# Performance work log

Hardware: AMD Instinct MI355X
Metric: run time of the kernel (lower is better)

The kernel has to match this reference:

```python
import jax, jax.numpy as jnp
import numpy as np

N = 100000       # nodes
E = 1600000      # edges (before self loops)
G = 64           # graphs in batch
IN, HID, OUT = 128, 64, 16
NEG_SLOPE = 0.2  # PyG GATConv default


def setup_inputs() -> dict:
    key = jax.random.key(0)
    ks = jax.random.split(key, 16)
    s = 0.1  # weight init scale
    return {
        "x": jax.random.normal(ks[0], (N, IN), dtype=jnp.float32),
        "edge_index": jax.random.randint(ks[1], (2, E), 0, N, dtype=jnp.int32),
        "batch": jnp.sort(jax.random.randint(ks[2], (N,), 0, G, dtype=jnp.int32)),
        "W1": jax.random.normal(ks[3], (IN, 2 * HID), dtype=jnp.float32) * s,
        "a_src1": jax.random.normal(ks[4], (2, HID), dtype=jnp.float32) * s,
        "a_dst1": jax.random.normal(ks[5], (2, HID), dtype=jnp.float32) * s,
        "b1": jax.random.normal(ks[6], (2 * HID,), dtype=jnp.float32) * s,
        "W2": jax.random.normal(ks[7], (2 * HID, HID), dtype=jnp.float32) * s,
        "a_src2": jax.random.normal(ks[8], (1, HID), dtype=jnp.float32) * s,
        "a_dst2": jax.random.normal(ks[9], (1, HID), dtype=jnp.float32) * s,
        "b2": jax.random.normal(ks[10], (HID,), dtype=jnp.float32) * s,
        "dw1": jax.random.normal(ks[11], (HID, HID), dtype=jnp.float32) * s,
        "db1": jax.random.normal(ks[12], (HID,), dtype=jnp.float32) * s,
        "dw2": jax.random.normal(ks[13], (HID, OUT), dtype=jnp.float32) * s,
        "db2": jax.random.normal(ks[14], (OUT,), dtype=jnp.float32) * s,
    }


def gat_conv(x, src, dst, W, a_src, a_dst, b):
    """PyG GATConv (concat=True, self-loops already appended to src/dst)."""
    n = x.shape[0]
    heads, out = a_src.shape
    h = (x @ W).reshape(n, heads, out)                       # [N,H,O]
    e_src = jnp.einsum("nho,ho->nh", h, a_src)               # [N,H]
    e_dst = jnp.einsum("nho,ho->nh", h, a_dst)
    e = jax.nn.leaky_relu(e_src[src] + e_dst[dst], NEG_SLOPE)  # [E',H]
    # segment softmax over incoming edges of each destination node
    m = jax.lax.stop_gradient(jax.ops.segment_max(e, dst, num_segments=n))
    a = jnp.exp(e - m[dst])
    denom = jax.ops.segment_sum(a, dst, num_segments=n)
    alpha = a / denom[dst]                                   # [E',H]
    msg = h[src] * alpha[:, :, None]                         # [E',H,O]
    agg = jax.ops.segment_sum(msg, dst, num_segments=n)      # [N,H,O]
    return agg.reshape(n, heads * out) + b


def reference(x, edge_index, batch, W1, a_src1, a_dst1, b1, W2, a_src2, a_dst2,
              b2, dw1, db1, dw2, db2):
    n = x.shape[0]
    loops = jnp.arange(n, dtype=edge_index.dtype)            # add_self_loops=True
    src = jnp.concatenate([edge_index[0], loops])
    dst = jnp.concatenate([edge_index[1], loops])

    h = jax.nn.relu(gat_conv(x, src, dst, W1, a_src1, a_dst1, b1))   # [N,128]
    h = gat_conv(h, src, dst, W2, a_src2, a_dst2, b2)                # [N,64]

    # global mean pool over graphs
    cnt = jax.ops.segment_sum(jnp.ones((n,), h.dtype), batch, num_segments=G)
    pooled = jax.ops.segment_sum(h, batch, num_segments=G)
    pooled = pooled / jnp.maximum(cnt, 1.0)[:, None]                  # [G,64]

    # decoder MLP (dropout inactive in eval)
    z = jax.nn.relu(pooled @ dw1 + db1)
    return z @ dw2 + db2                                              # [G,16]
```

## Files before the change

### kernel.cpp

```cpp
#include <hip/hip_runtime.h>
#include <stdint.h>


#define LRELU(x) ((x) > 0.f ? (x) : 0.2f * (x))
#define LOG2E 1.4426950408889634f
#define BCAP 3072
#define PSLICE 8

typedef short bf8 __attribute__((ext_vector_type(8)));
typedef float f32x4 __attribute__((ext_vector_type(4)));
typedef float f32x2 __attribute__((ext_vector_type(2)));

__device__ __forceinline__ uint16_t f2bf(float f) {
  uint32_t u = __float_as_uint(f);
  u += 0x7fff + ((u >> 16) & 1);
  return (uint16_t)(u >> 16);
}
__device__ __forceinline__ uint32_t pack2bf(float a, float b) {
  return (uint32_t)f2bf(a) | ((uint32_t)f2bf(b) << 16);
}
__device__ __forceinline__ uint8_t f2fp8(float v) {
  return (uint8_t)(__builtin_amdgcn_cvt_pk_fp8_f32(v, v, 0, false) & 0xff);
}
__device__ __forceinline__ void fp8x4_to_f32(uint32_t v, float* o) {
  f32x2 lo = __builtin_amdgcn_cvt_pk_f32_fp8(v, false);
  f32x2 hi = __builtin_amdgcn_cvt_pk_f32_fp8(v, true);
  o[0] = lo[0]; o[1] = lo[1]; o[2] = hi[0]; o[3] = hi[1];
}
__device__ __forceinline__ void a1_edge(const uint4& gv, float av, float* acc) {
  float f[16];
  fp8x4_to_f32(gv.x, f);     fp8x4_to_f32(gv.y, f + 4);
  fp8x4_to_f32(gv.z, f + 8); fp8x4_to_f32(gv.w, f + 12);
#pragma unroll
  for (int j = 0; j < 16; ++j) acc[j] = fmaf(av, f[j], acc[j]);
}
__device__ __forceinline__ void a2_edge(const uint2& gv, float av, float* acc) {
  float f[8];
  fp8x4_to_f32(gv.x, f); fp8x4_to_f32(gv.y, f + 4);
#pragma unroll
  for (int j = 0; j < 8; ++j) acc[j] = fmaf(av, f[j], acc[j]);
}


__global__ __launch_bounds__(256) void scatter_cvt_kernel(
    const int* __restrict__ ei, int* __restrict__ bcur,
    uint32_t* __restrict__ bpack, const float* __restrict__ W1,
    const float* __restrict__ W2, uint16_t* __restrict__ WT1,
    uint16_t* __restrict__ WT2, int E, int E2, int shift, int nb, int gCH) {
  int blk = blockIdx.x;
  int t = threadIdx.x;
  if (blk >= gCH) {
    int idx = (blk - gCH) * 256 + t;
    if (idx < 128 * 128) {
      int n = idx >> 7, k = idx & 127;
      WT1[idx] = f2bf(W1[(size_t)k * 128 + n]);
    } else if (idx < 128 * 128 + 64 * 128) {
      int j = idx - 128 * 128;
      int n = j >> 7, k = j & 127;
      WT2[j] = f2bf(W2[(size_t)k * 64 + n]);
    }
    return;
  }
  __shared__ int lh[1024];
  __shared__ int lb[1024];
  for (int i = t; i < 1024; i += 256) lh[i] = 0;
  __syncthreads();
  int base = blk * 4096;
  int bszm1 = (1 << shift) - 1;
  uint32_t pk[16];
  int rk[16], bk[16];
#pragma unroll
  for (int u = 0; u < 16; ++u) {
    int e = base + u * 256 + t;
    if (e < E2) {
      int s, d;
      if (e < E) { s = ei[e]; d = ei[E + e]; } else { s = d = e - E; }
      bk[u] = d >> shift;
      pk[u] = ((uint32_t)s << shift) | (uint32_t)(d & bszm1);
      rk[u] = atomicAdd(&lh[bk[u]], 1);
    } else rk[u] = -1;
  }
  __syncthreads();
  for (int i = t; i < nb; i += 256) {
    int c = lh[i];
    lb[i] = c ? atomicAdd(&bcur[i], c) : 0;
  }
  __syncthreads();
#pragma unroll
  for (int u = 0; u < 16; ++u) {
    if (rk[u] >= 0) {
      int pos = lb[bk[u]] + rk[u];
      if (pos < BCAP) bpack[(size_t)bk[u] * BCAP + pos] = pk[u];
    }
  }
}


__device__ __forceinline__ void bfinal_body(const uint32_t* __restrict__ bpack,
                                            const int* __restrict__ bcur,
                                            int2* __restrict__ off2,
                                            int* __restrict__ ssrc, int N,
                                            int shift, int b) {
  __shared__ int hist[512];
  __shared__ int loff[512];
  __shared__ int ssc[256];
  __shared__ int lsrc[BCAP];
  int t = threadIdx.x;
  int bsz = 1 << shift;
  int node0 = b << shift;
  int e0 = b * BCAP;
  int cnt = min(bcur[b], BCAP);
  for (int i = t; i < bsz; i += 256) hist[i] = 0;
  __syncthreads();
  uint32_t pe[12];
  int ne = 0;
#pragma unroll
  for (int j = 0; j < 12; ++j) {
    int i = j * 256 + t;
    if (i < cnt) { pe[j] = bpack[(size_t)b * BCAP + i]; ne = j + 1; }
  }
  int bszm1 = bsz - 1;
  for (int j = 0; j < ne; ++j) atomicAdd(&hist[pe[j] & bszm1], 1);
  __syncthreads();
  int per = (bsz + 255) >> 8;
  int basei = t * per;
  int va[2] = {0, 0};
  int sum = 0;
#pragma unroll 2
  for (int j = 0; j < per; ++j) {
    if (basei + j < bsz) va[j] = hist[basei + j];
    sum += va[j];
  }
  ssc[t] = sum;
  __syncthreads();
  for (int d = 1; d < 256; d <<= 1) {
    int x = (t >= d) ? ssc[t - d] : 0;
    __syncthreads();
    ssc[t] += x;
    __syncthreads();
  }
  int run = ssc[t] - sum;
#pragma unroll 2
  for (int j = 0; j < per; ++j) {
    if (basei + j < bsz) {
      loff[basei + j] = run;
      int v = node0 + basei + j;
      if (v < N) off2[v] = make_int2(e0 + run, e0 + run + va[j]);
      run += va[j];
    }
  }
  for (int i = t; i < bsz; i += 256) hist[i] = 0;
  __syncthreads();
  for (int j = 0; j < ne; ++j) {
    int ld = pe[j] & bszm1;
    int r = atomicAdd(&hist[ld], 1);
    lsrc[loff[ld] + r] = (int)(pe[j] >> shift);
  }
  __syncthreads();
  for (int i = t; i < cnt; i += 256) ssrc[e0 + i] = lsrc[i];
}


template <int N, int HEADS, int AFP32>
__device__ __forceinline__ void gemm_body(const void* __restrict__ Av,
                                          const uint16_t* __restrict__ WT,
                                          uint8_t* __restrict__ C,
                                          const float* __restrict__ aS,
                                          const float* __restrict__ aD,
                                          float* __restrict__ es,
                                          float* __restrict__ ed, int M, int blk) {
  constexpr int CT = N / 16;
  int wave = threadIdx.x >> 6;
  int lane = threadIdx.x & 63;
  int m16 = lane & 15;
  int quad = lane >> 4;
  int row_base = blk * 128 + wave * 32;
  if (row_base >= M) return;
  const uint16_t* Ab0 = (const uint16_t*)Av + (size_t)(row_base + m16) * 128;
  const uint16_t* Ab1 = Ab0 + (size_t)16 * 128;
  const float* Af0 = (const float*)Av + (size_t)(row_base + m16) * 128;
  const float* Af1 = Af0 + (size_t)16 * 128;
  f32x4 acc[2][CT] = {};
#pragma unroll
  for (int ks = 0; ks < 4; ++ks) {
    int k0 = ks * 32 + quad * 8;
    bf8 a0, a1;
    if (AFP32) {
      float4 v0 = *reinterpret_cast<const float4*>(Af0 + k0);
      float4 v1 = *reinterpret_cast<const float4*>(Af0 + k0 + 4);
      uint4 pk0;
      pk0.x = pack2bf(v0.x, v0.y); pk0.y = pack2bf(v0.z, v0.w);
      pk0.z = pack2bf(v1.x, v1.y); pk0.w = pack2bf(v1.z, v1.w);
      a0 = *reinterpret_cast<bf8*>(&pk0);
      float4 w0 = *reinterpret_cast<const float4*>(Af1 + k0);
      float4 w1 = *reinterpret_cast<const float4*>(Af1 + k0 + 4);
      uint4 pk1;
      pk1.x = pack2bf(w0.x, w0.y); pk1.y = pack2bf(w0.z, w0.w);
      pk1.z = pack2bf(w1.x, w1.y); pk1.w = pack2bf(w1.z, w1.w);
      a1 = *reinterpret_cast<bf8*>(&pk1);
    } else {
      a0 = *reinterpret_cast<const bf8*>(Ab0 + k0);
      a1 = *reinterpret_cast<const bf8*>(Ab1 + k0);
    }
#pragma unroll
    for (int c = 0; c < CT; ++c) {
      bf8 b = *reinterpret_cast<const bf8*>(WT + (size_t)(c * 16 + m16) * 128 + k0);
      acc[0][c] = __builtin_amdgcn_mfma_f32_16x16x32_bf16(a0, b, acc[0][c], 0, 0, 0);
      acc[1][c] = __builtin_amdgcn_mfma_f32_16x16x32_bf16(a1, b, acc[1][c], 0, 0, 0);
    }
  }
#pragma unroll
  for (int r = 0; r < 2; ++r) {
#pragma unroll
    for (int c = 0; c < CT; ++c) {
#pragma unroll
      for (int reg = 0; reg < 4; ++reg) {
        int row = row_base + r * 16 + quad * 4 + reg;
        C[(size_t)row * N + c * 16 + m16] = f2fp8(acc[r][c][reg]);
      }
    }
  }
  float aSv[CT], aDv[CT];
#pragma unroll
  for (int c = 0; c < CT; ++c) {
    aSv[c] = aS[c * 16 + m16];
    aDv[c] = aD[c * 16 + m16];
  }
#pragma unroll
  for (int r = 0; r < 2; ++r) {
#pragma unroll
    for (int reg = 0; reg < 4; ++reg) {
      float es0 = 0.f, es1 = 0.f, ed0 = 0.f, ed1 = 0.f;
#pragma unroll
      for (int c = 0; c < CT; ++c) {
        float v = acc[r][c][reg];
        if (HEADS == 2 && c >= CT / 2) {
          es1 = fmaf(v, aSv[c], es1);
          ed1 = fmaf(v, aDv[c], ed1);
        } else {
          es0 = fmaf(v, aSv[c], es0);
          ed0 = fmaf(v, aDv[c], ed0);
        }
      }
#pragma unroll
      for (int o = 1; o < 16; o <<= 1) {
        es0 += __shfl_xor(es0, o);
        ed0 += __shfl_xor(ed0, o);
        if (HEADS == 2) {
          es1 += __shfl_xor(es1, o);
          ed1 += __shfl_xor(ed1, o);
        }
      }
      if (m16 == 0) {
        int row = row_base + r * 16 + quad * 4 + reg;
        if (HEADS == 2) {
          es[row * 2] = es0 * LOG2E; es[row * 2 + 1] = es1 * LOG2E;
          ed[row * 2] = ed0 * LOG2E; ed[row * 2 + 1] = ed1 * LOG2E;
        } else {
          es[row] = es0 * LOG2E;
          ed[row] = ed0 * LOG2E;
        }
      }
    }
  }
}


__global__ __launch_bounds__(256) void gemm1_bfinal_kernel(
    const float* __restrict__ x, const uint16_t* __restrict__ WT1,
    uint8_t* __restrict__ hb1, const float* __restrict__ aS,
    const float* __restrict__ aD, float* __restrict__ es, float* __restrict__ ed,
    int M, const uint32_t* __restrict__ bpack, const int* __restrict__ bcur,
    int2* __restrict__ off2, int* __restrict__ ssrc, int shift, int gM) {
  int blk = blockIdx.x;
  if (blk < gM) {
    gemm_body<128, 2, 1>(x, WT1, hb1, aS, aD, es, ed, M, blk);
  } else {
    bfinal_body(bpack, bcur, off2, ssrc, M, shift, blk - gM);
  }
}

template <int N, int HEADS, int AFP32>
__global__ __launch_bounds__(256) void gemm_mfma(const void* __restrict__ Av,
                                                 const uint16_t* __restrict__ WT,
                                                 uint8_t* __restrict__ C,
                                                 const float* __restrict__ aS,
                                                 const float* __restrict__ aD,
                                                 float* __restrict__ es,
                                                 float* __restrict__ ed, int M) {
  gemm_body<N, HEADS, AFP32>(Av, WT, C, aS, aD, es, ed, M, blockIdx.x);
}


__global__ void agg1_kernel(const uint4* __restrict__ h16, const float* __restrict__ es,
                            const float2* __restrict__ ed, const int2* __restrict__ off2,
                            const int* __restrict__ ssrc, const float* __restrict__ b,
                            uint4* __restrict__ outb4, int n) {
  int wv = __builtin_amdgcn_readfirstlane((blockIdx.x * 256 + threadIdx.x) >> 6);
  int lane = threadIdx.x & 63;
  int grp = lane >> 3;
  int cl = lane & 7;
  int w = wv * 8 + grp;
  if (w >= n) return;
  bool hi = cl >= 4;
  float2 edw = ed[w];
  float edh = hi ? edw.y : edw.x;
  const float* esp = es + (hi ? 1 : 0);
  float acc[16] = {};
  float den = 0.f;
  int2 oo = off2[w];
  int e = oo.x, e1 = oo.y;
  for (; e + 4 <= e1; e += 4) {
    int s0 = ssrc[e];
    int s1 = ssrc[e + 1];
    int s2 = ssrc[e + 2];
    int s3 = ssrc[e + 3];
    uint4 g0 = h16[(size_t)s0 * 8 + cl];
    uint4 g1 = h16[(size_t)s1 * 8 + cl];
    uint4 g2 = h16[(size_t)s2 * 8 + cl];
    uint4 g3 = h16[(size_t)s3 * 8 + cl];
    float a0 = exp2f(LRELU(esp[2 * s0] + edh));
    float a1 = exp2f(LRELU(esp[2 * s1] + edh));
    float a2 = exp2f(LRELU(esp[2 * s2] + edh));
    float a3 = exp2f(LRELU(esp[2 * s3] + edh));
    den += (a0 + a1) + (a2 + a3);
    a1_edge(g0, a0, acc);
    a1_edge(g1, a1, acc);
    a1_edge(g2, a2, acc);
    a1_edge(g3, a3, acc);
  }
  for (; e < e1; ++e) {
    int s0 = ssrc[e];
    uint4 g0 = h16[(size_t)s0 * 8 + cl];
    float a0 = exp2f(LRELU(esp[2 * s0] + edh));
    den += a0;
    a1_edge(g0, a0, acc);
  }
  float inv = 1.0f / den;
  float o[16];
#pragma unroll
  for (int k = 0; k < 4; ++k) {
    float4 bb = reinterpret_cast<const float4*>(b)[cl * 4 + k];
    o[k * 4 + 0] = fmaxf(fmaf(acc[k * 4 + 0], inv, bb.x), 0.f);
    o[k * 4 + 1] = fmaxf(fmaf(acc[k * 4 + 1], inv, bb.y), 0.f);
    o[k * 4 + 2] = fmaxf(fmaf(acc[k * 4 + 2], inv, bb.z), 0.f);
    o[k * 4 + 3] = fmaxf(fmaf(acc[k * 4 + 3], inv, bb.w), 0.f);
  }
  uint4 oA, oB;
  oA.x = pack2bf(o[0], o[1]);   oA.y = pack2bf(o[2], o[3]);
  oA.z = pack2bf(o[4], o[5]);   oA.w = pack2bf(o[6], o[7]);
  oB.x = pack2bf(o[8], o[9]);   oB.y = pack2bf(o[10], o[11]);
  oB.z = pack2bf(o[12], o[13]); oB.w = pack2bf(o[14], o[15]);
  outb4[(size_t)w * 16 + cl * 2] = oA;
  outb4[(size_t)w * 16 + cl * 2 + 1] = oB;
}


__global__ void agg2_pool_kernel(const uint2* __restrict__ h8,
                                 const float* __restrict__ es,
                                 const float* __restrict__ ed,
                                 const int2* __restrict__ off2,
                                 const int* __restrict__ ssrc,
                                 const float* __restrict__ b,
                                 const int* __restrict__ batch,
                                 float* __restrict__ pooled, int gstride, int n) {
  int t = threadIdx.x;
  int wv = __builtin_amdgcn_readfirstlane((blockIdx.x * 256 + t) >> 6);
  int wave = t >> 6;
  int lane = t & 63;
  int grp = lane >> 3;
  int cl = lane & 7;
  int w = wv * 8 + grp;
  bool act = (w < n);
  __shared__ float red[4][64];
  __shared__ int uniS[4];
  float* pslice = pooled + (size_t)(blockIdx.x & (PSLICE - 1)) * gstride;
  float acc[8] = {};
  int g = -1;
  if (act) {
    g = batch[w];
    float edw = ed[w];
    float den = 0.f;
    int2 oo = off2[w];
    int e = oo.x, e1 = oo.y;
    for (; e + 4 <= e1; e += 4) {
      int s0 = ssrc[e];
      int s1 = ssrc[e + 1];
      int s2 = ssrc[e + 2];
      int s3 = ssrc[e + 3];
      uint2 g0 = h8[(size_t)s0 * 8 + cl];
      uint2 g1 = h8[(size_t)s1 * 8 + cl];
      uint2 g2 = h8[(size_t)s2 * 8 + cl];
      uint2 g3 = h8[(size_t)s3 * 8 + cl];
      float a0 = exp2f(LRELU(es[s0] + edw));
      float a1 = exp2f(LRELU(es[s1] + edw));
      float a2 = exp2f(LRELU(es[s2] + edw));
      float a3 = exp2f(LRELU(es[s3] + edw));
      den += (a0 + a1) + (a2 + a3);
      a2_edge(g0, a0, acc);
      a2_edge(g1, a1, acc);
      a2_edge(g2, a2, acc);
      a2_edge(g3, a3, acc);
    }
    for (; e < e1; ++e) {
      int s0 = ssrc[e];
      uint2 g0 = h8[(size_t)s0 * 8 + cl];
      float a0 = exp2f(LRELU(es[s0] + edw));
      den += a0;
      a2_edge(g0, a0, acc);
    }
    float inv = 1.0f / den;
    float4 b0 = reinterpret_cast<const float4*>(b)[cl * 2];
    float4 b1 = reinterpret_cast<const float4*>(b)[cl * 2 + 1];
    acc[0] = fmaf(acc[0], inv, b0.x);
    acc[1] = fmaf(acc[1], inv, b0.y);
    acc[2] = fmaf(acc[2], inv, b0.z);
    acc[3] = fmaf(acc[3], inv, b0.w);
    acc[4] = fmaf(acc[4], inv, b1.x);
    acc[5] = fmaf(acc[5], inv, b1.y);
    acc[6] = fmaf(acc[6], inv, b1.z);
    acc[7] = fmaf(acc[7], inv, b1.w);
  }
  int g0lane = __shfl(g, 0);
  bool same = __all(g == g0lane);
  if (same && g0lane >= 0) {
#pragma unroll
    for (int m = 8; m <= 32; m <<= 1) {
#pragma unroll
      for (int j = 0; j < 8; ++j) acc[j] += __shfl_xor(acc[j], m);
    }
    if (grp == 0) {
#pragma unroll
      for (int j = 0; j < 8; ++j) red[wave][cl * 8 + j] = acc[j];
    }
    if (lane == 0) uniS[wave] = g0lane;
  } else {
    if (lane == 0) uniS[wave] = same ? -1 : -2;
    if (act && !same) {
#pragma unroll
      for (int j = 0; j < 8; ++j)
        atomicAdd(&pslice[(size_t)g * 64 + cl * 8 + j], acc[j]);
    }
  }
  __syncthreads();
  int u0 = uniS[0];
  bool allsame = (u0 >= 0) & (uniS[1] == u0) & (uniS[2] == u0) & (uniS[3] == u0);
  if (allsame) {
    if (t < 64) {
      float s = red[0][t] + red[1][t] + red[2][t] + red[3][t];
      atomicAdd(&pslice[(size_t)u0 * 64 + t], s);
    }
  } else {
    int gw = uniS[wave];
    if (gw >= 0) atomicAdd(&pslice[(size_t)gw * 64 + lane], red[wave][lane]);
  }
}


__device__ __forceinline__ int lowerb(const int* __restrict__ a, int n, int v) {
  int lo = 0, hi = n;
  while (lo < hi) {
    int mid = (lo + hi) >> 1;
    if (a[mid] < v) lo = mid + 1; else hi = mid;
  }
  return lo;
}

__global__ void mlp_kernel(const float* __restrict__ pooled, int gstride,
                           const int* __restrict__ batch, int n,
                           const float* __restrict__ dw1, const float* __restrict__ db1,
                           const float* __restrict__ dw2, const float* __restrict__ db2,
                           float* __restrict__ out) {
  int g = blockIdx.x;
  int c = threadIdx.x;
  __shared__ float P[64];
  __shared__ float Z[64];
  __shared__ int cntS;
  if (c == 0) cntS = lowerb(batch, n, g + 1) - lowerb(batch, n, g);
  __syncthreads();
  float inv = 1.0f / fmaxf((float)cntS, 1.0f);
  float p = 0.f;
#pragma unroll
  for (int s = 0; s < PSLICE; ++s) p += pooled[(size_t)s * gstride + g * 64 + c];
  P[c] = p * inv;
  __syncthreads();
  float s = db1[c];
#pragma unroll
  for (int k = 0; k < 64; ++k) s = fmaf(P[k], dw1[k * 64 + c], s);
  Z[c] = fmaxf(s, 0.f);
  __syncthreads();
  if (c < 16) {
    float s2 = db2[c];
#pragma unroll
    for (int k = 0; k < 64; ++k) s2 = fmaf(Z[k], dw2[k * 16 + c], s2);
    out[g * 16 + c] = s2;
  }
}


extern "C" void kernel_launch(void* const* d_in, const int* in_sizes, int n_in,
                              void* d_out, int out_size, void* d_ws, size_t ws_size,
                              hipStream_t stream) {
  const float* x      = (const float*)d_in[0];
  const int*   ei     = (const int*)d_in[1];
  const int*   batch  = (const int*)d_in[2];
  const float* W1     = (const float*)d_in[3];
  const float* a_src1 = (const float*)d_in[4];
  const float* a_dst1 = (const float*)d_in[5];
  const float* b1     = (const float*)d_in[6];
  const float* W2     = (const float*)d_in[7];
  const float* a_src2 = (const float*)d_in[8];
  const float* a_dst2 = (const float*)d_in[9];
  const float* b2     = (const float*)d_in[10];
  const float* dw1    = (const float*)d_in[11];
  const float* db1    = (const float*)d_in[12];
  const float* dw2    = (const float*)d_in[13];
  const float* db2    = (const float*)d_in[14];
  float* out = (float*)d_out;

  const int N = in_sizes[2];
  const int E = in_sizes[1] / 2;
  const int E2 = E + N;
  const int G = out_size / 16;
  const int gstride = G * 64;

  int shift = 7;
  while ((N >> shift) >= 1024) ++shift;
  const int NB = ((N - 1) >> shift) + 1;

  char* ws = (char*)d_ws;
  size_t o = 0;
  auto alloc = [&](size_t bytes) {
    void* p = ws + o;
    o = (o + bytes + 255) & ~(size_t)255;
    return p;
  };
  int*      zreg   = (int*)alloc((size_t)(1024 + PSLICE * gstride) * 4);
  int*      bcur   = zreg;
  float*    pooled = (float*)(zreg + 1024);
  int2*     off2   = (int2*)alloc((size_t)N * 8);
  uint32_t* bpack  = (uint32_t*)alloc((size_t)NB * BCAP * 4);
  int*      ssrc   = (int*)alloc((size_t)NB * BCAP * 4);
  float*    es1    = (float*)alloc((size_t)N * 2 * 4);
  float*    ed1    = (float*)alloc((size_t)N * 2 * 4);
  float*    es2    = (float*)alloc((size_t)N * 4);
  float*    ed2    = (float*)alloc((size_t)N * 4);
  uint16_t* wt1b   = (uint16_t*)alloc((size_t)128 * 128 * 2);
  uint16_t* wt2b   = (uint16_t*)alloc((size_t)64 * 128 * 2);
  uint8_t*  hb1    = (uint8_t*)alloc((size_t)N * 128);
  uint8_t*  hb2    = (uint8_t*)alloc((size_t)N * 64);
  uint32_t* out1b  = (uint32_t*)alloc((size_t)N * 64 * 4);

  hipMemsetAsync(zreg, 0, (size_t)(1024 + PSLICE * gstride) * 4, stream);

  int gM   = (N + 127) / 128;
  int gW   = (N + 31) / 32;
  int gCH  = (E2 + 4095) / 4096;
  int gCVT = (128 * 128 + 64 * 128 + 255) / 256;

  scatter_cvt_kernel<<<gCH + gCVT, 256, 0, stream>>>(ei, bcur, bpack, W1, W2,
                                                     wt1b, wt2b, E, E2, shift,
                                                     NB, gCH);
  gemm1_bfinal_kernel<<<gM + NB, 256, 0, stream>>>(x, wt1b, hb1, a_src1, a_dst1,
                                                   es1, ed1, N, bpack, bcur,
                                                   off2, ssrc, shift, gM);
  agg1_kernel<<<gW, 256, 0, stream>>>((const uint4*)hb1, es1,
                                      (const float2*)ed1, off2, ssrc, b1,
                                      (uint4*)out1b, N);
  gemm_mfma<64, 1, 0><<<gM, 256, 0, stream>>>((const void*)out1b, wt2b, hb2,
                                              a_src2, a_dst2, es2, ed2, N);
  agg2_pool_kernel<<<gW, 256, 0, stream>>>((const uint2*)hb2, es2, ed2, off2,
                                           ssrc, b2, batch, pooled, gstride, N);
  mlp_kernel<<<G, 64, 0, stream>>>(pooled, gstride, batch, N, dw1, db1, dw2,
                                   db2, out);
}
```

Baseline: 264.5 us.

## Sort nodes by in-degree within buckets to balance aggregation waves

During CSR finalisation, each bucket counting-sorts its nodes by in-degree (capped at 63) into a permutation array. Both aggregation kernels then process nodes in permuted order, so the 8 nodes sharing a wave have similar edge counts. This targets divergence where a wave waits for its highest-degree node. In exchange it adds an indirection load, scatters the per-node output writes, and may split pooling runs of same-graph nodes.

```diff
diff --git a/kernel.cpp b/kernel.cpp
--- a/kernel.cpp
+++ b/kernel.cpp
@@ -99,11 +99,13 @@
 __device__ __forceinline__ void bfinal_body(const uint32_t* __restrict__ bpack,
                                             const int* __restrict__ bcur,
                                             int2* __restrict__ off2,
-                                            int* __restrict__ ssrc, int N,
+                                            int* __restrict__ ssrc,
+                                            int* __restrict__ perm, int N,
                                             int shift, int b) {
   __shared__ int hist[512];
   __shared__ int loff[512];
   __shared__ int ssc[256];
+  __shared__ int dbin[65];
   __shared__ int lsrc[BCAP];
   int t = threadIdx.x;
   int bsz = 1 << shift;
@@ -111,6 +113,7 @@
   int e0 = b * BCAP;
   int cnt = min(bcur[b], BCAP);
   for (int i = t; i < bsz; i += 256) hist[i] = 0;
+  if (t < 65) dbin[t] = 0;
   __syncthreads();
   uint32_t pe[12];
   int ne = 0;
@@ -140,13 +143,39 @@
     __syncthreads();
   }
   int run = ssc[t] - sum;
+  int dc[2] = {0, 0};
 #pragma unroll 2
   for (int j = 0; j < per; ++j) {
     if (basei + j < bsz) {
       loff[basei + j] = run;
       int v = node0 + basei + j;
-      if (v < N) off2[v] = make_int2(e0 + run, e0 + run + va[j]);
+      if (v < N) {
+        off2[v] = make_int2(e0 + run, e0 + run + va[j]);
+        dc[j] = min(va[j], 63);
+        atomicAdd(&dbin[dc[j]], 1);
+      }
       run += va[j];
+    }
+  }
+  __syncthreads();
+  if (t < 64) {
+    int v = dbin[t], s = v;
+#pragma unroll
+    for (int d2 = 1; d2 < 64; d2 <<= 1) {
+      int u = __shfl_up(s, d2);
+      if (t >= d2) s += u;
+    }
+    dbin[t] = s - v;
+  }
+  __syncthreads();
+#pragma unroll 2
+  for (int j = 0; j < per; ++j) {
+    if (basei + j < bsz) {
+      int v = node0 + basei + j;
+      if (v < N) {
+        int r = atomicAdd(&dbin[dc[j]], 1);
+        perm[node0 + r] = v;
+      }
     }
   }
   for (int i = t; i < bsz; i += 256) hist[i] = 0;
@@ -271,12 +300,13 @@
     uint8_t* __restrict__ hb1, const float* __restrict__ aS,
     const float* __restrict__ aD, float* __restrict__ es, float* __restrict__ ed,
     int M, const uint32_t* __restrict__ bpack, const int* __restrict__ bcur,
-    int2* __restrict__ off2, int* __restrict__ ssrc, int shift, int gM) {
+    int2* __restrict__ off2, int* __restrict__ ssrc, int* __restrict__ perm,
+    int shift, int gM) {
   int blk = blockIdx.x;
   if (blk < gM) {
     gemm_body<128, 2, 1>(x, WT1, hb1, aS, aD, es, ed, M, blk);
   } else {
-    bfinal_body(bpack, bcur, off2, ssrc, M, shift, blk - gM);
+    bfinal_body(bpack, bcur, off2, ssrc, perm, M, shift, blk - gM);
   }
 }
 
@@ -294,14 +324,16 @@
 
 __global__ void agg1_kernel(const uint4* __restrict__ h16, const float* __restrict__ es,
                             const float2* __restrict__ ed, const int2* __restrict__ off2,
-                            const int* __restrict__ ssrc, const float* __restrict__ b,
+                            const int* __restrict__ ssrc, const int* __restrict__ perm,
+                            const float* __restrict__ b,
                             uint4* __restrict__ outb4, int n) {
   int wv = __builtin_amdgcn_readfirstlane((blockIdx.x * 256 + threadIdx.x) >> 6);
   int lane = threadIdx.x & 63;
   int grp = lane >> 3;
   int cl = lane & 7;
-  int w = wv * 8 + grp;
-  if (w >= n) return;
+  int idx = wv * 8 + grp;
+  if (idx >= n) return;
+  int w = perm[idx];
   bool hi = cl >= 4;
   float2 edw = ed[w];
   float edh = hi ? edw.y : edw.x;
@@ -361,6 +393,7 @@
                                  const float* __restrict__ ed,
                                  const int2* __restrict__ off2,
                                  const int* __restrict__ ssrc,
+                                 const int* __restrict__ perm,
                                  const float* __restrict__ b,
                                  const int* __restrict__ batch,
                                  float* __restrict__ pooled, int gstride, int n) {
@@ -370,8 +403,9 @@
   int lane = t & 63;
   int grp = lane >> 3;
   int cl = lane & 7;
-  int w = wv * 8 + grp;
-  bool act = (w < n);
+  int idx = wv * 8 + grp;
+  bool act = (idx < n);
+  int w = act ? perm[idx] : 0;
   __shared__ float red[4][64];
   __shared__ int uniS[4];
   float* pslice = pooled + (size_t)(blockIdx.x & (PSLICE - 1)) * gstride;
@@ -539,6 +573,7 @@
   int*      bcur   = zreg;
   float*    pooled = (float*)(zreg + 1024);
   int2*     off2   = (int2*)alloc((size_t)N * 8);
+  int*      perm   = (int*)alloc((size_t)N * 4);
   uint32_t* bpack  = (uint32_t*)alloc((size_t)NB * BCAP * 4);
   int*      ssrc   = (int*)alloc((size_t)NB * BCAP * 4);
   float*    es1    = (float*)alloc((size_t)N * 2 * 4);
@@ -563,14 +598,15 @@
                                                      NB, gCH);
   gemm1_bfinal_kernel<<<gM + NB, 256, 0, stream>>>(x, wt1b, hb1, a_src1, a_dst1,
                                                    es1, ed1, N, bpack, bcur,
-                                                   off2, ssrc, shift, gM);
+                                                   off2, ssrc, perm, shift, gM);
   agg1_kernel<<<gW, 256, 0, stream>>>((const uint4*)hb1, es1,
-                                      (const float2*)ed1, off2, ssrc, b1,
+                                      (const float2*)ed1, off2, ssrc, perm, b1,
                                       (uint4*)out1b, N);
   gemm_mfma<64, 1, 0><<<gM, 256, 0, stream>>>((const void*)out1b, wt2b, hb2,
                                               a_src2, a_dst2, es2, ed2, N);
   agg2_pool_kernel<<<gW, 256, 0, stream>>>((const uint2*)hb2, es2, ed2, off2,
-                                           ssrc, b2, batch, pooled, gstride, N);
+                                           ssrc, perm, b2, batch, pooled,
+                                           gstride, N);
   mlp_kernel<<<G, 64, 0, stream>>>(pooled, gstride, batch, N, dw1, db1, dw2,
                                    db2, out);
 }
```

Measured after the change: 313.6 us. +18.6%, slower.

## Fuse layer-1 aggregation with layer-2 GEMM through swizzled shared memory

Applied to the files above, without the earlier changes.

Layer-1 edge aggregation and the layer-2 MFMA GEMM now run in a single kernel. Each 256-thread block aggregates 128 destination nodes into a swizzled 32KB LDS tile of bf16 features, then runs the 128x64 GEMM directly from LDS and computes the layer-2 attention logits. This removes the intermediate 25MB bf16 buffer write and read-back and one kernel launch. In exchange each block does four sequential aggregation rounds per wave and uses 32KB of LDS, which lowers occupancy and latency hiding for the gather-bound aggregation.

```diff
diff --git a/kernel.cpp b/kernel.cpp
--- a/kernel.cpp
+++ b/kernel.cpp
@@ -176,10 +176,10 @@
   int quad = lane >> 4;
   int row_base = blk * 128 + wave * 32;
   if (row_base >= M) return;
+  const float* Af0 = (const float*)Av + (size_t)(row_base + m16) * 128;
+  const float* Af1 = Af0 + (size_t)16 * 128;
   const uint16_t* Ab0 = (const uint16_t*)Av + (size_t)(row_base + m16) * 128;
   const uint16_t* Ab1 = Ab0 + (size_t)16 * 128;
-  const float* Af0 = (const float*)Av + (size_t)(row_base + m16) * 128;
-  const float* Af1 = Af0 + (size_t)16 * 128;
   f32x4 acc[2][CT] = {};
 #pragma unroll
   for (int ks = 0; ks < 4; ++ks) {
@@ -280,79 +280,141 @@
   }
 }
 
-template <int N, int HEADS, int AFP32>
-__global__ __launch_bounds__(256) void gemm_mfma(const void* __restrict__ Av,
-                                                 const uint16_t* __restrict__ WT,
-                                                 uint8_t* __restrict__ C,
-                                                 const float* __restrict__ aS,
-                                                 const float* __restrict__ aD,
-                                                 float* __restrict__ es,
-                                                 float* __restrict__ ed, int M) {
-  gemm_body<N, HEADS, AFP32>(Av, WT, C, aS, aD, es, ed, M, blockIdx.x);
-}
-
-
-__global__ void agg1_kernel(const uint4* __restrict__ h16, const float* __restrict__ es,
-                            const float2* __restrict__ ed, const int2* __restrict__ off2,
-                            const int* __restrict__ ssrc, const float* __restrict__ b,
-                            uint4* __restrict__ outb4, int n) {
-  int wv = __builtin_amdgcn_readfirstlane((blockIdx.x * 256 + threadIdx.x) >> 6);
-  int lane = threadIdx.x & 63;
+
+__global__ __launch_bounds__(256) void agg1_gemm2_kernel(
+    const uint4* __restrict__ h16, const float* __restrict__ es1,
+    const float2* __restrict__ ed1, const int2* __restrict__ off2,
+    const int* __restrict__ ssrc, const float* __restrict__ b1,
+    const uint16_t* __restrict__ WT2, uint8_t* __restrict__ hb2,
+    const float* __restrict__ aS, const float* __restrict__ aD,
+    float* __restrict__ es2, float* __restrict__ ed2, int n) {
+  __shared__ uint32_t Abuf[128 * 64];
+  int t = threadIdx.x;
+  int wave = t >> 6;
+  int lane = t & 63;
   int grp = lane >> 3;
   int cl = lane & 7;
-  int w = wv * 8 + grp;
-  if (w >= n) return;
   bool hi = cl >= 4;
-  float2 edw = ed[w];
-  float edh = hi ? edw.y : edw.x;
-  const float* esp = es + (hi ? 1 : 0);
-  float acc[16] = {};
-  float den = 0.f;
-  int2 oo = off2[w];
-  int e = oo.x, e1 = oo.y;
-  for (; e + 4 <= e1; e += 4) {
-    int s0 = ssrc[e];
-    int s1 = ssrc[e + 1];
-    int s2 = ssrc[e + 2];
-    int s3 = ssrc[e + 3];
-    uint4 g0 = h16[(size_t)s0 * 8 + cl];
-    uint4 g1 = h16[(size_t)s1 * 8 + cl];
-    uint4 g2 = h16[(size_t)s2 * 8 + cl];
-    uint4 g3 = h16[(size_t)s3 * 8 + cl];
-    float a0 = exp2f(LRELU(esp[2 * s0] + edh));
-    float a1 = exp2f(LRELU(esp[2 * s1] + edh));
-    float a2 = exp2f(LRELU(esp[2 * s2] + edh));
-    float a3 = exp2f(LRELU(esp[2 * s3] + edh));
-    den += (a0 + a1) + (a2 + a3);
-    a1_edge(g0, a0, acc);
-    a1_edge(g1, a1, acc);
-    a1_edge(g2, a2, acc);
-    a1_edge(g3, a3, acc);
-  }
-  for (; e < e1; ++e) {
-    int s0 = ssrc[e];
-    uint4 g0 = h16[(size_t)s0 * 8 + cl];
-    float a0 = exp2f(LRELU(esp[2 * s0] + edh));
-    den += a0;
-    a1_edge(g0, a0, acc);
-  }
-  float inv = 1.0f / den;
-  float o[16];
-#pragma unroll
-  for (int k = 0; k < 4; ++k) {
-    float4 bb = reinterpret_cast<const float4*>(b)[cl * 4 + k];
-    o[k * 4 + 0] = fmaxf(fmaf(acc[k * 4 + 0], inv, bb.x), 0.f);
-    o[k * 4 + 1] = fmaxf(fmaf(acc[k * 4 + 1], inv, bb.y), 0.f);
-    o[k * 4 + 2] = fmaxf(fmaf(acc[k * 4 + 2], inv, bb.z), 0.f);
-    o[k * 4 + 3] = fmaxf(fmaf(acc[k * 4 + 3], inv, bb.w), 0.f);
-  }
-  uint4 oA, oB;
-  oA.x = pack2bf(o[0], o[1]);   oA.y = pack2bf(o[2], o[3]);
-  oA.z = pack2bf(o[4], o[5]);   oA.w = pack2bf(o[6], o[7]);
-  oB.x = pack2bf(o[8], o[9]);   oB.y = pack2bf(o[10], o[11]);
-  oB.z = pack2bf(o[12], o[13]); oB.w = pack2bf(o[14], o[15]);
-  outb4[(size_t)w * 16 + cl * 2] = oA;
-  outb4[(size_t)w * 16 + cl * 2 + 1] = oB;
+  int blk = blockIdx.x;
+  for (int r = 0; r < 4; ++r) {
+    int wl = wave * 32 + r * 8 + grp;
+    int w = blk * 128 + wl;
+    if (w < n) {
+      float2 edw = ed1[w];
+      float edh = hi ? edw.y : edw.x;
+      const float* esp = es1 + (hi ? 1 : 0);
+      float acc[16] = {};
+      float den = 0.f;
+      int2 oo = off2[w];
+      int e = oo.x, e1 = oo.y;
+      for (; e + 4 <= e1; e += 4) {
+        int s0 = ssrc[e];
+        int s1 = ssrc[e + 1];
+        int s2 = ssrc[e + 2];
+        int s3 = ssrc[e + 3];
+        uint4 g0 = h16[(size_t)s0 * 8 + cl];
+        uint4 g1 = h16[(size_t)s1 * 8 + cl];
+        uint4 g2 = h16[(size_t)s2 * 8 + cl];
+        uint4 g3 = h16[(size_t)s3 * 8 + cl];
+        float a0 = exp2f(LRELU(esp[2 * s0] + edh));
+        float a1 = exp2f(LRELU(esp[2 * s1] + edh));
+        float a2 = exp2f(LRELU(esp[2 * s2] + edh));
+        float a3 = exp2f(LRELU(esp[2 * s3] + edh));
+        den += (a0 + a1) + (a2 + a3);
+        a1_edge(g0, a0, acc);
+        a1_edge(g1, a1, acc);
+        a1_edge(g2, a2, acc);
+        a1_edge(g3, a3, acc);
+      }
+      for (; e < e1; ++e) {
+        int s0 = ssrc[e];
+        uint4 g0 = h16[(size_t)s0 * 8 + cl];
+        float a0 = exp2f(LRELU(esp[2 * s0] + edh));
+        den += a0;
+        a1_edge(g0, a0, acc);
+      }
+      float inv = 1.0f / den;
+      float o[16];
+#pragma unroll
+      for (int k = 0; k < 4; ++k) {
+        float4 bb = reinterpret_cast<const float4*>(b1)[cl * 4 + k];
+        o[k * 4 + 0] = fmaxf(fmaf(acc[k * 4 + 0], inv, bb.x), 0.f);
+        o[k * 4 + 1] = fmaxf(fmaf(acc[k * 4 + 1], inv, bb.y), 0.f);
+        o[k * 4 + 2] = fmaxf(fmaf(acc[k * 4 + 2], inv, bb.z), 0.f);
+        o[k * 4 + 3] = fmaxf(fmaf(acc[k * 4 + 3], inv, bb.w), 0.f);
+      }
+      uint4 oA, oB;
+      oA.x = pack2bf(o[0], o[1]);   oA.y = pack2bf(o[2], o[3]);
+      oA.z = pack2bf(o[4], o[5]);   oA.w = pack2bf(o[6], o[7]);
+      oB.x = pack2bf(o[8], o[9]);   oB.y = pack2bf(o[10], o[11]);
+      oB.z = pack2bf(o[12], o[13]); oB.w = pack2bf(o[14], o[15]);
+      int swz = (wl & 7) << 2;
+      *reinterpret_cast<uint4*>(&Abuf[wl * 64 + ((cl * 8) ^ swz)]) = oA;
+      *reinterpret_cast<uint4*>(&Abuf[wl * 64 + ((cl * 8 + 4) ^ swz)]) = oB;
+    }
+  }
+  __syncthreads();
+  int m16 = lane & 15;
+  int quad = lane >> 4;
+  int row_base = blk * 128 + wave * 32;
+  if (row_base >= n) return;
+  int rl0 = wave * 32 + m16;
+  int rl1 = rl0 + 16;
+  int swz0 = (m16 & 7) << 2;
+  f32x4 acc2[2][4] = {};
+#pragma unroll
+  for (int ks = 0; ks < 4; ++ks) {
+    int c32 = ks * 16 + quad * 4;
+    bf8 a0 = *reinterpret_cast<const bf8*>(&Abuf[rl0 * 64 + (c32 ^ swz0)]);
+    bf8 a1 = *reinterpret_cast<const bf8*>(&Abuf[rl1 * 64 + (c32 ^ swz0)]);
+    int k0 = ks * 32 + quad * 8;
+#pragma unroll
+    for (int c = 0; c < 4; ++c) {
+      bf8 b = *reinterpret_cast<const bf8*>(WT2 + (size_t)(c * 16 + m16) * 128 + k0);
+      acc2[0][c] = __builtin_amdgcn_mfma_f32_16x16x32_bf16(a0, b, acc2[0][c], 0, 0, 0);
+      acc2[1][c] = __builtin_amdgcn_mfma_f32_16x16x32_bf16(a1, b, acc2[1][c], 0, 0, 0);
+    }
+  }
+#pragma unroll
+  for (int rr = 0; rr < 2; ++rr) {
+#pragma unroll
+    for (int c = 0; c < 4; ++c) {
+#pragma unroll
+      for (int reg = 0; reg < 4; ++reg) {
+        int row = row_base + rr * 16 + quad * 4 + reg;
+        hb2[(size_t)row * 64 + c * 16 + m16] = f2fp8(acc2[rr][c][reg]);
+      }
+    }
+  }
+  float aSv[4], aDv[4];
+#pragma unroll
+  for (int c = 0; c < 4; ++c) {
+    aSv[c] = aS[c * 16 + m16];
+    aDv[c] = aD[c * 16 + m16];
+  }
+#pragma unroll
+  for (int rr = 0; rr < 2; ++rr) {
+#pragma unroll
+    for (int reg = 0; reg < 4; ++reg) {
+      float e0 = 0.f, d0 = 0.f;
+#pragma unroll
+      for (int c = 0; c < 4; ++c) {
+        float v = acc2[rr][c][reg];
+        e0 = fmaf(v, aSv[c], e0);
+        d0 = fmaf(v, aDv[c], d0);
+      }
+#pragma unroll
+      for (int o = 1; o < 16; o <<= 1) {
+        e0 += __shfl_xor(e0, o);
+        d0 += __shfl_xor(d0, o);
+      }
+      if (m16 == 0) {
+        int row = row_base + rr * 16 + quad * 4 + reg;
+        es2[row] = e0 * LOG2E;
+        ed2[row] = d0 * LOG2E;
+      }
+    }
+  }
 }
 
 
@@ -492,7 +554,7 @@
   if (c < 16) {
     float s2 = db2[c];
 #pragma unroll
-    for (int k = 0; k < 64; ++k) s2 = fmaf(Z[k], dw2[k * 16 + c], s2);
+    for (int c2 = 0; c2 < 64; ++c2) s2 = fmaf(Z[c2], dw2[c2 * 16 + c], s2);
     out[g * 16 + c] = s2;
   }
 }
@@ -549,7 +611,6 @@
   uint16_t* wt2b   = (uint16_t*)alloc((size_t)64 * 128 * 2);
   uint8_t*  hb1    = (uint8_t*)alloc((size_t)N * 128);
   uint8_t*  hb2    = (uint8_t*)alloc((size_t)N * 64);
-  uint32_t* out1b  = (uint32_t*)alloc((size_t)N * 64 * 4);
 
   hipMemsetAsync(zreg, 0, (size_t)(1024 + PSLICE * gstride) * 4, stream);
 
@@ -564,11 +625,10 @@
   gemm1_bfinal_kernel<<<gM + NB, 256, 0, stream>>>(x, wt1b, hb1, a_src1, a_dst1,
                                                    es1, ed1, N, bpack, bcur,
                                                    off2, ssrc, shift, gM);
-  agg1_kernel<<<gW, 256, 0, stream>>>((const uint4*)hb1, es1,
-                                      (const float2*)ed1, off2, ssrc, b1,
-                                      (uint4*)out1b, N);
-  gemm_mfma<64, 1, 0><<<gM, 256, 0, stream>>>((const void*)out1b, wt2b, hb2,
-                                              a_src2, a_dst2, es2, ed2, N);
+  agg1_gemm2_kernel<<<gM, 256, 0, stream>>>((const uint4*)hb1, es1,
+                                            (const float2*)ed1, off2, ssrc, b1,
+                                            wt2b, hb2, a_src2, a_dst2,
+                                            es2, ed2, N);
   agg2_pool_kernel<<<gW, 256, 0, stream>>>((const uint2*)hb2, es2, ed2, off2,
                                            ssrc, b2, batch, pooled, gstride, N);
   mlp_kernel<<<G, 64, 0, stream>>>(pooled, gstride, batch, N, dw1, db1, dw2,
```

After: 278.8 us. +5.4%, slower.
